# Kernel optimization log

Hardware: AMD Instinct MI355X
Metric: run time of the kernel (lower is better)

Reference implementation:

```python
import jax, jax.numpy as jnp
import numpy as np

D_MODEL = 1024
NUM_HEADS = 16
NUM_KV_HEADS = 4
D_K = D_MODEL // NUM_HEADS              # 64
G = NUM_HEADS // NUM_KV_HEADS           # queries per kv head = 4
B, S = 2, 2048


def setup_inputs() -> dict:
    key = jax.random.key(0)
    ks = jax.random.split(key, 11)
    s = 0.02
    return {
        "query": jax.random.normal(ks[0], (B, S, D_MODEL), jnp.float32),
        "key_in": jax.random.normal(ks[1], (B, S, D_MODEL), jnp.float32),
        "value_in": jax.random.normal(ks[2], (B, S, D_MODEL), jnp.float32),
        "Wq": jax.random.normal(ks[3], (D_MODEL, D_MODEL), jnp.float32) * s,
        "bq": jnp.zeros((D_MODEL,), jnp.float32),
        "Wk": jax.random.normal(ks[4], (D_MODEL, NUM_KV_HEADS * D_K), jnp.float32) * s,
        "bk": jnp.zeros((NUM_KV_HEADS * D_K,), jnp.float32),
        "Wv": jax.random.normal(ks[5], (D_MODEL, NUM_KV_HEADS * D_K), jnp.float32) * s,
        "bv": jnp.zeros((NUM_KV_HEADS * D_K,), jnp.float32),
        "Wo": jax.random.normal(ks[6], (D_MODEL, D_MODEL), jnp.float32) * s,
        "bo": jnp.zeros((D_MODEL,), jnp.float32),
    }


def reference(query, key_in, value_in, Wq, bq, Wk, bk, Wv, bv, Wo, bo):
    scale = jnp.sqrt(jnp.asarray(D_K, query.dtype))
    # Projections
    Q = (query @ Wq + bq).reshape(B, S, NUM_HEADS, D_K).transpose(0, 2, 1, 3)        # [B,H,S,dk]
    K = (key_in @ Wk + bk).reshape(B, S, NUM_KV_HEADS, D_K).transpose(0, 2, 1, 3)    # [B,KVH,S,dk]
    V = (value_in @ Wv + bv).reshape(B, S, NUM_KV_HEADS, D_K).transpose(0, 2, 1, 3)  # [B,KVH,S,dk]
    # repeat_interleave over head dim -> group Q heads by KV head instead
    Qg = Q.reshape(B, NUM_KV_HEADS, G, S, D_K)                                       # [B,KVH,G,S,dk]
    scores = jnp.einsum('bkgqd,bksd->bkgqs', Qg, K) / scale                          # [B,KVH,G,S,S]
    attn = jax.nn.softmax(scores, axis=-1)
    ctx = jnp.einsum('bkgqs,bksd->bkgqd', attn, V)                                   # [B,KVH,G,S,dk]
    ctx = ctx.reshape(B, NUM_HEADS, S, D_K).transpose(0, 2, 1, 3).reshape(B, S, D_MODEL)
    output = ctx @ Wo + bo
    # new_cache: K[:, ::G] on the repeated tensor == original K/V per kv head
    return output, K, V
```

## Files before the change

kernel.cpp:

```cpp
#include <hip/hip_runtime.h>

typedef unsigned short u16;
typedef unsigned int u32;
typedef __attribute__((ext_vector_type(8))) short short8;
typedef __attribute__((ext_vector_type(4))) float f32x4;

#define MFMA16(a, b, c) __builtin_amdgcn_mfma_f32_16x16x32_bf16(a, b, c, 0, 0, 0)

#define SEQ 2048
#define DM 1024

__device__ __forceinline__ u16 f2bf(float f) {
  u32 u = __float_as_uint(f);
  u += 0x7fffu + ((u >> 16) & 1u);
  return (u16)(u >> 16);
}
__device__ __forceinline__ u32 pack2(float a, float b) {
  u32 r;
  asm("v_cvt_pk_bf16_f32 %0, %1, %2" : "=v"(r) : "v"(a), "v"(b));
  return r;
}
__device__ __forceinline__ u32 pack2t(float a, float b) {
  return __builtin_amdgcn_perm(__float_as_uint(b), __float_as_uint(a), 0x07060302u);
}
__device__ __forceinline__ void pswap32(u32& a, u32& b) {
  asm("v_permlane32_swap_b32 %0, %1" : "+v"(a), "+v"(b));
}
__device__ __forceinline__ void pswap16(u32& a, u32& b) {
  asm("v_permlane16_swap_b32 %0, %1" : "+v"(a), "+v"(b));
}
__device__ __forceinline__ uint4 cvt8(const float* f) {
  float4 a = *(const float4*)f;
  float4 b = *(const float4*)(f + 4);
  uint4 r;
  r.x = pack2(a.x, a.y);
  r.y = pack2(a.z, a.w);
  r.z = pack2(b.x, b.y);
  r.w = pack2(b.z, b.w);
  return r;
}
__device__ __forceinline__ void gload16(const u16* g, u16* l) {
  __builtin_amdgcn_global_load_lds((const __attribute__((address_space(1))) u32*)g,
                                   (__attribute__((address_space(3))) u32*)l, 16, 0, 0);
}

__global__ void k_tr(const float* __restrict__ Wq, const float* __restrict__ Wk,
                     const float* __restrict__ Wv, const float* __restrict__ Wo,
                     u16* __restrict__ WqT, u16* __restrict__ WkT, u16* __restrict__ WvT,
                     u16* __restrict__ WoT) {
  const int z = blockIdx.z;
  const float* W = z == 0 ? Wq : (z == 1 ? Wk : (z == 2 ? Wv : Wo));
  u16* Wt = z == 0 ? WqT : (z == 1 ? WkT : (z == 2 ? WvT : WoT));
  const int N = (z == 1 || z == 2) ? 256 : 1024;
  const int n0 = blockIdx.x * 32;
  if (n0 >= N) return;
  const int k0 = blockIdx.y * 32;
  __shared__ float tile[32][33];
  int x = threadIdx.x & 31, y = threadIdx.x >> 5;
#pragma unroll
  for (int i = 0; i < 4; i++)
    tile[y + i * 8][x] = W[(size_t)(k0 + y + i * 8) * N + n0 + x];
  __syncthreads();
#pragma unroll
  for (int i = 0; i < 4; i++)
    Wt[(size_t)(n0 + y + i * 8) * 1024 + k0 + x] = f2bf(tile[x][y + i * 8]);
}

template <bool A32, bool B32>
__device__ __forceinline__ void gemm64(const void* __restrict__ A, const void* __restrict__ Bt,
                                       int m0, int n0, u16* lA, u16* lB, f32x4 acc[2][4]) {
  const int tid = threadIdx.x;
  const int lane = tid & 63, wave = tid >> 6;
  const int l15 = lane & 15, quad = lane >> 4;
  const int wm = wave >> 1, wn = wave & 1;
  const int sr = tid >> 3, scol = (tid & 7) * 8;
  f32x4 zero = {0.f, 0.f, 0.f, 0.f};
#pragma unroll
  for (int i = 0; i < 2; i++)
#pragma unroll
    for (int j = 0; j < 4; j++) acc[i][j] = zero;

  for (int k0 = 0; k0 < 1024; k0 += 64) {
    if constexpr (A32) {
      const float* Af = (const float*)A;
#pragma unroll
      for (int it = 0; it < 2; it++) {
        int r = sr + it * 32;
        uint4 v = cvt8(Af + (size_t)(m0 + r) * 1024 + k0 + scol);
        *(uint4*)&lA[r * 64 + (((tid & 7) ^ (r & 7)) << 3)] = v;
      }
    } else {
      const u16* Ab = (const u16*)A;
#pragma unroll
      for (int it = 0; it < 2; it++) {
        int w8 = wave * 2 + it;
        int r = w8 * 8 + (lane >> 3);
        int g = (lane & 7) ^ (lane >> 3);
        gload16(Ab + (size_t)(m0 + r) * 1024 + k0 + g * 8, &lA[w8 * 512]);
      }
    }
    if constexpr (B32) {
      const float* Bf = (const float*)Bt;
#pragma unroll
      for (int it = 0; it < 4; it++) {
        int r = sr + it * 32;
        uint4 v = cvt8(Bf + (size_t)(n0 + r) * 1024 + k0 + scol);
        *(uint4*)&lB[r * 64 + (((tid & 7) ^ (r & 7)) << 3)] = v;
      }
    } else {
      const u16* Bb = (const u16*)Bt;
#pragma unroll
      for (int it = 0; it < 4; it++) {
        int w8 = wave * 4 + it;
        int r = w8 * 8 + (lane >> 3);
        int g = (lane & 7) ^ (lane >> 3);
        gload16(Bb + (size_t)(n0 + r) * 1024 + k0 + g * 8, &lB[w8 * 512]);
      }
    }
    __syncthreads();
    short8 af[2][2], bfr[4][2];
#pragma unroll
    for (int i = 0; i < 2; i++)
#pragma unroll
      for (int kb = 0; kb < 2; kb++) {
        int r = wm * 32 + i * 16 + l15;
        af[i][kb] = *(const short8*)&lA[r * 64 + (((kb * 4 + quad) ^ (r & 7)) << 3)];
      }
#pragma unroll
    for (int j = 0; j < 4; j++)
#pragma unroll
      for (int kb = 0; kb < 2; kb++) {
        int r = wn * 64 + j * 16 + l15;
        bfr[j][kb] = *(const short8*)&lB[r * 64 + (((kb * 4 + quad) ^ (r & 7)) << 3)];
      }
#pragma unroll
    for (int i = 0; i < 2; i++)
#pragma unroll
      for (int j = 0; j < 4; j++) {
        acc[i][j] = MFMA16(af[i][0], bfr[j][0], acc[i][j]);
        acc[i][j] = MFMA16(af[i][1], bfr[j][1], acc[i][j]);
      }
    __syncthreads();
  }
}

__global__ __launch_bounds__(256) void k_proj(
    const float* __restrict__ query, const float* __restrict__ key_in,
    const float* __restrict__ value_in, const u16* __restrict__ WqT,
    const u16* __restrict__ WkT, const u16* __restrict__ WvT, const float* __restrict__ bq,
    const float* __restrict__ bk, const float* __restrict__ bv, u16* __restrict__ qbf,
    float* __restrict__ outK, u16* __restrict__ kbf, float* __restrict__ outV,
    u16* __restrict__ vtb, float qscale) {
  __shared__ u16 lA[64 * 64];
  __shared__ u16 lB[128 * 64];
  const int idx = blockIdx.x;
  const int lane = threadIdx.x & 63, wave = threadIdx.x >> 6;
  const int l15 = lane & 15, quad = lane >> 4;
  const int wm = wave >> 1, wn = wave & 1;
  f32x4 acc[2][4];

  if (idx < 640) {
    const u16* Wt;
    const float* act;
    const float* bias;
    int m0, n0, mode;
    if (idx < 512) {
      Wt = WqT; act = query; bias = bq; m0 = (idx >> 5) * 64; n0 = (idx & 31) * 128; mode = 0;
    } else {
      int i2 = idx - 512;
      Wt = WkT; act = key_in; bias = bk; m0 = (i2 >> 5) * 64; n0 = (i2 & 31) * 128; mode = 1;
    }
    gemm64<false, true>(Wt, act, m0, n0, lA, lB, acc);
#pragma unroll
    for (int i = 0; i < 2; i++) {
      int c0 = m0 + wm * 32 + i * 16 + quad * 4;
      float4 bb = *(const float4*)(bias + c0);
#pragma unroll
      for (int j = 0; j < 4; j++) {
        int token = n0 + wn * 64 + j * 16 + l15;
        int b = token >> 11, s = token & 2047;
        float v0 = acc[i][j][0] + bb.x, v1 = acc[i][j][1] + bb.y;
        float v2 = acc[i][j][2] + bb.z, v3 = acc[i][j][3] + bb.w;
        int d = c0 & 63;
        if (mode == 0) {
          int h = c0 >> 6;
          uint2 o;
          o.x = pack2(v0 * qscale, v1 * qscale);
          o.y = pack2(v2 * qscale, v3 * qscale);
          *(uint2*)(qbf + (((size_t)(b * 16 + h) * SEQ + s) << 6) + d) = o;
        } else {
          int kvh = c0 >> 6;
          size_t ix = (((size_t)(b * 4 + kvh) * SEQ + s) << 6) + d;
          float4 vv = {v0, v1, v2, v3};
          *(float4*)(outK + ix) = vv;
          uint2 o;
          o.x = pack2(v0, v1);
          o.y = pack2(v2, v3);
          *(uint2*)(kbf + ix) = o;
        }
      }
    }
  } else {
    int i2 = idx - 640;
    int m0 = (i2 >> 1) * 64, n0 = (i2 & 1) * 128;
    gemm64<true, false>(value_in, WvT, m0, n0, lA, lB, acc);
#pragma unroll
    for (int i = 0; i < 2; i++) {
      int r0 = m0 + wm * 32 + i * 16 + quad * 4;
      int b = r0 >> 11, s0 = r0 & 2047;
#pragma unroll
      for (int j = 0; j < 4; j++) {
        int col = n0 + wn * 64 + j * 16 + l15;
        int kvh = col >> 6, d = col & 63;
        float bv_ = bv[col];
        float v0 = acc[i][j][0] + bv_, v1 = acc[i][j][1] + bv_;
        float v2 = acc[i][j][2] + bv_, v3 = acc[i][j][3] + bv_;
        size_t base = (((size_t)(b * 4 + kvh) * SEQ + s0) << 6) + d;
        outV[base] = v0;
        outV[base + 64] = v1;
        outV[base + 128] = v2;
        outV[base + 192] = v3;
        uint2 o;
        o.x = pack2(v0, v1);
        o.y = pack2(v2, v3);
        *(uint2*)(vtb + ((size_t)(b * 4 + kvh) * 64 + d) * SEQ + s0) = o;
      }
    }
  }
}

__global__ __launch_bounds__(256) void k_out(const u16* __restrict__ ctxb,
                                             const u16* __restrict__ WoT,
                                             const float* __restrict__ bo,
                                             float* __restrict__ out) {
  __shared__ u16 lA[64 * 64];
  __shared__ u16 lB[128 * 64];
  const int idx = blockIdx.x;
  const int m0 = (idx >> 5) * 64, n0 = (idx & 31) * 128;
  const int lane = threadIdx.x & 63, wave = threadIdx.x >> 6;
  const int l15 = lane & 15, quad = lane >> 4;
  const int wm = wave >> 1, wn = wave & 1;
  f32x4 acc[2][4];
  gemm64<false, false>(WoT, ctxb, m0, n0, lA, lB, acc);
#pragma unroll
  for (int i = 0; i < 2; i++) {
    int c0 = m0 + wm * 32 + i * 16 + quad * 4;
    float4 bb = *(const float4*)(bo + c0);
#pragma unroll
    for (int j = 0; j < 4; j++) {
      int token = n0 + wn * 64 + j * 16 + l15;
      float4 vv = {acc[i][j][0] + bb.x, acc[i][j][1] + bb.y, acc[i][j][2] + bb.z,
                   acc[i][j][3] + bb.w};
      *(float4*)(out + (size_t)token * DM + c0) = vv;
    }
  }
}

__global__ __launch_bounds__(256, 2) void k_flash(const u16* __restrict__ Qh,
                                                  const u16* __restrict__ Kb,
                                                  const u16* __restrict__ Vt,
                                                  u16* __restrict__ ctx) {
  __shared__ u16 lK[2][128 * 64];
  __shared__ u16 lV[2][64 * 128];
  const int tid = threadIdx.x;
  const int lane = tid & 63, wave = tid >> 6;
  const int l15 = lane & 15, quad = lane >> 4;
  const int bh = blockIdx.y;
  const int b = bh >> 4, h = bh & 15, kvh = h >> 2;
  const u16* Q = Qh + (size_t)bh * SEQ * 64;
  const u16* Kp = Kb + (size_t)(b * 4 + kvh) * SEQ * 64;
  const u16* Vp = Vt + (size_t)(b * 4 + kvh) * 64 * SEQ;
  const int q0 = blockIdx.x * 128 + wave * 32;

  short8 qf[2][2];
#pragma unroll
  for (int g = 0; g < 2; g++)
#pragma unroll
    for (int kb = 0; kb < 2; kb++)
      qf[g][kb] = *(const short8*)(Q + (size_t)(q0 + g * 16 + l15) * 64 + kb * 32 + quad * 8);

  short8 ones8;
  {
    short ov = (l15 == 0) ? (short)0x3F80 : (short)0;
    ones8 = (short8){ov, ov, ov, ov, ov, ov, ov, ov};
  }

  f32x4 zero = {0.f, 0.f, 0.f, 0.f};
  f32x4 acc[2][4];
  f32x4 lacc[2] = {zero, zero};
#pragma unroll
  for (int g = 0; g < 2; g++)
#pragma unroll
    for (int n = 0; n < 4; n++) acc[g][n] = zero;

  const int gr3 = lane >> 3, gc7 = lane & 7;
  const int gr4 = lane >> 4, gc15 = lane & 15;

  auto stage = [&](int kc, int bufi) {
    u16* dK = lK[bufi];
    u16* dV = lV[bufi];
#pragma unroll
    for (int i = 0; i < 4; i++) {
      int slab = wave * 4 + i;
      gload16(Kp + (size_t)(kc + slab * 8 + gr3) * 64 + ((gc7 ^ gr3) << 3), dK + slab * 512);
    }
#pragma unroll
    for (int i = 0; i < 4; i++) {
      int slab = wave * 4 + i;
      int row = slab * 4 + gr4;
      gload16(Vp + (size_t)row * SEQ + kc + ((gc15 ^ (row & 15)) << 3), dV + slab * 512);
    }
  };

  stage(0, 0);
  __syncthreads();

  for (int t = 0; t < SEQ / 128; t++) {
    if (t < SEQ / 128 - 1) stage((t + 1) * 128, (t + 1) & 1);
    const u16* cK = lK[t & 1];
    const u16* cV = lV[t & 1];

#pragma unroll
    for (int sub = 0; sub < 2; sub++) {
      const int ks = sub * 64;
      f32x4 sc[2][4];
#pragma unroll
      for (int mt = 0; mt < 4; mt++) {
        int row = ks + mt * 16 + l15;
        short8 kf0 = *(const short8*)&cK[row * 64 + ((quad ^ (row & 7)) << 3)];
        short8 kf1 = *(const short8*)&cK[row * 64 + (((4 + quad) ^ (row & 7)) << 3)];
#pragma unroll
        for (int g = 0; g < 2; g++) {
          f32x4 t0 = MFMA16(kf0, qf[g][0], zero);
          sc[g][mt] = MFMA16(kf1, qf[g][1], t0);
        }
      }
#pragma unroll
      for (int g = 0; g < 2; g++)
#pragma unroll
        for (int mt = 0; mt < 4; mt++)
#pragma unroll
          for (int r = 0; r < 4; r++) sc[g][mt][r] = __builtin_amdgcn_exp2f(sc[g][mt][r]);

#pragma unroll
      for (int kbp = 0; kbp < 2; kbp++) {
        short8 pf[2];
#pragma unroll
        for (int g = 0; g < 2; g++) {
          u32 U0 = pack2t(sc[g][2 * kbp][0], sc[g][2 * kbp][1]);
          u32 W0 = pack2t(sc[g][2 * kbp + 1][0], sc[g][2 * kbp + 1][1]);
          u32 U1 = pack2t(sc[g][2 * kbp][2], sc[g][2 * kbp][3]);
          u32 W1 = pack2t(sc[g][2 * kbp + 1][2], sc[g][2 * kbp + 1][3]);
          pswap32(U0, W0);
          pswap16(U0, W0);
          pswap32(U1, W1);
          pswap16(U1, W1);
          u32 w[4] = {U0, U1, W0, W1};
          pf[g] = *(const short8*)w;
        }
        lacc[0] = MFMA16(ones8, pf[0], lacc[0]);
        lacc[1] = MFMA16(ones8, pf[1], lacc[1]);
#pragma unroll
        for (int n = 0; n < 4; n++) {
          int row = n * 16 + l15;
          int chv = sub * 8 + kbp * 4 + quad;
          short8 vf = *(const short8*)&cV[row * 128 + ((chv ^ (row & 15)) << 3)];
          acc[0][n] = MFMA16(vf, pf[0], acc[0][n]);
          acc[1][n] = MFMA16(vf, pf[1], acc[1][n]);
        }
      }
    }
    __syncthreads();
  }

#pragma unroll
  for (int g = 0; g < 2; g++) {
    float lq = __shfl(lacc[g][0], l15);
    float inv = __builtin_amdgcn_rcpf(lq);
    u16* base = ctx + ((size_t)(b * SEQ + q0 + g * 16 + l15)) * DM + h * 64;
#pragma unroll
    for (int n = 0; n < 4; n++) {
      uint2 o;
      o.x = pack2t(acc[g][n][0] * inv, acc[g][n][1] * inv);
      o.y = pack2t(acc[g][n][2] * inv, acc[g][n][3] * inv);
      *(uint2*)(base + n * 16 + quad * 4) = o;
    }
  }
}

extern "C" void kernel_launch(void* const* d_in, const int* in_sizes, int n_in,
                              void* d_out, int out_size, void* d_ws, size_t ws_size,
                              hipStream_t stream) {
  const float* query = (const float*)d_in[0];
  const float* key_in = (const float*)d_in[1];
  const float* value_in = (const float*)d_in[2];
  const float* Wq = (const float*)d_in[3];
  const float* bq = (const float*)d_in[4];
  const float* Wk = (const float*)d_in[5];
  const float* bk = (const float*)d_in[6];
  const float* Wv = (const float*)d_in[7];
  const float* bv = (const float*)d_in[8];
  const float* Wo = (const float*)d_in[9];
  const float* bo = (const float*)d_in[10];

  float* out = (float*)d_out;
  float* outK = out + 4194304;
  float* outV = out + 5242880;

  char* ws = (char*)d_ws;
  u16* WqT = (u16*)(ws);
  u16* WkT = (u16*)(ws + 2097152);
  u16* WvT = (u16*)(ws + 2621440);
  u16* WoT = (u16*)(ws + 3145728);
  u16* qbf = (u16*)(ws + 5242880);
  u16* kbf = (u16*)(ws + 13631488);
  u16* vtb = (u16*)(ws + 15728640);
  u16* ctxb = (u16*)(ws + 17825792);

  const float qscale = 0.125f * 1.44269504088896340736f;

  k_tr<<<dim3(32, 32, 4), 256, 0, stream>>>(Wq, Wk, Wv, Wo, WqT, WkT, WvT, WoT);
  k_proj<<<dim3(768), 256, 0, stream>>>(query, key_in, value_in, WqT, WkT, WvT, bq, bk, bv,
                                        qbf, outK, kbf, outV, vtb, qscale);
  k_flash<<<dim3(16, 32), 256, 0, stream>>>(qbf, kbf, vtb, ctxb);
  k_out<<<dim3(512), 256, 0, stream>>>(ctxb, WoT, bo, out);
}
```

Baseline: 200.1 us.

## Fuse weight transpose into GEMM loads and double-buffer LDS tiles

Drops the separate weight transpose/bf16-convert kernel. The projection and output GEMMs now read fp32 weights directly with strided loads, converting and transposing them while writing to LDS. The GEMM main loop is also double-buffered: the next tile's global loads go into registers before the MFMAs on the current tile, and are written to LDS afterwards. This saves one launch and one pass over the weights, at the cost of more registers, twice the LDS, and less coalesced weight reads, since each lane reads one column across rows.

```diff
diff --git a/kernel.cpp b/kernel.cpp
--- a/kernel.cpp
+++ b/kernel.cpp
@@ -10,11 +10,6 @@
 #define SEQ 2048
 #define DM 1024
 
-__device__ __forceinline__ u16 f2bf(float f) {
-  u32 u = __float_as_uint(f);
-  u += 0x7fffu + ((u >> 16) & 1u);
-  return (u16)(u >> 16);
-}
 __device__ __forceinline__ u32 pack2(float a, float b) {
   u32 r;
   asm("v_cvt_pk_bf16_f32 %0, %1, %2" : "=v"(r) : "v"(a), "v"(b));
@@ -29,109 +24,152 @@
 __device__ __forceinline__ void pswap16(u32& a, u32& b) {
   asm("v_permlane16_swap_b32 %0, %1" : "+v"(a), "+v"(b));
 }
-__device__ __forceinline__ uint4 cvt8(const float* f) {
-  float4 a = *(const float4*)f;
-  float4 b = *(const float4*)(f + 4);
-  uint4 r;
-  r.x = pack2(a.x, a.y);
-  r.y = pack2(a.z, a.w);
-  r.z = pack2(b.x, b.y);
-  r.w = pack2(b.z, b.w);
-  return r;
-}
 __device__ __forceinline__ void gload16(const u16* g, u16* l) {
   __builtin_amdgcn_global_load_lds((const __attribute__((address_space(1))) u32*)g,
                                    (__attribute__((address_space(3))) u32*)l, 16, 0, 0);
 }
 
-__global__ void k_tr(const float* __restrict__ Wq, const float* __restrict__ Wk,
-                     const float* __restrict__ Wv, const float* __restrict__ Wo,
-                     u16* __restrict__ WqT, u16* __restrict__ WkT, u16* __restrict__ WvT,
-                     u16* __restrict__ WoT) {
-  const int z = blockIdx.z;
-  const float* W = z == 0 ? Wq : (z == 1 ? Wk : (z == 2 ? Wv : Wo));
-  u16* Wt = z == 0 ? WqT : (z == 1 ? WkT : (z == 2 ? WvT : WoT));
-  const int N = (z == 1 || z == 2) ? 256 : 1024;
-  const int n0 = blockIdx.x * 32;
-  if (n0 >= N) return;
-  const int k0 = blockIdx.y * 32;
-  __shared__ float tile[32][33];
-  int x = threadIdx.x & 31, y = threadIdx.x >> 5;
-#pragma unroll
-  for (int i = 0; i < 4; i++)
-    tile[y + i * 8][x] = W[(size_t)(k0 + y + i * 8) * N + n0 + x];
-  __syncthreads();
-#pragma unroll
-  for (int i = 0; i < 4; i++)
-    Wt[(size_t)(n0 + y + i * 8) * 1024 + k0 + x] = f2bf(tile[x][y + i * 8]);
-}
-
-template <bool A32, bool B32>
-__device__ __forceinline__ void gemm64(const void* __restrict__ A, const void* __restrict__ Bt,
-                                       int m0, int n0, u16* lA, u16* lB, f32x4 acc[2][4]) {
+#define MBF 0
+#define MF32 1
+#define MTR 2
+
+template <int AM, int BM>
+__device__ __forceinline__ void gemm64(const void* __restrict__ A, const void* __restrict__ B,
+                                       int m0, int n0, int ldA, int ldB, u16* lA, u16* lB,
+                                       f32x4 acc[2][4]) {
   const int tid = threadIdx.x;
   const int lane = tid & 63, wave = tid >> 6;
   const int l15 = lane & 15, quad = lane >> 4;
   const int wm = wave >> 1, wn = wave & 1;
-  const int sr = tid >> 3, scol = (tid & 7) * 8;
+  const int sr = tid >> 3, sch = tid & 7;
+  const int gr = lane >> 3, gch = (lane & 7) ^ (lane >> 3);
+  const int nb = tid & 127, ko = tid >> 7;
   f32x4 zero = {0.f, 0.f, 0.f, 0.f};
 #pragma unroll
   for (int i = 0; i < 2; i++)
 #pragma unroll
     for (int j = 0; j < 4; j++) acc[i][j] = zero;
 
-  for (int k0 = 0; k0 < 1024; k0 += 64) {
-    if constexpr (A32) {
-      const float* Af = (const float*)A;
+  float rA[16], rB[32];
+
+  auto issue = [&](int k0, u16* dA, u16* dB) {
+    if constexpr (AM == MBF) {
+#pragma unroll
+      for (int it = 0; it < 2; it++) {
+        int w8 = wave * 2 + it;
+        gload16((const u16*)A + (size_t)(m0 + w8 * 8 + gr) * ldA + k0 + gch * 8,
+                dA + w8 * 512);
+      }
+    } else if constexpr (AM == MF32) {
+#pragma unroll
+      for (int it = 0; it < 2; it++) {
+        const float* p = (const float*)A + (size_t)(m0 + sr + it * 32) * ldA + k0 + sch * 8;
+        float4 a = *(const float4*)p, b = *(const float4*)(p + 4);
+        rA[it * 8 + 0] = a.x; rA[it * 8 + 1] = a.y; rA[it * 8 + 2] = a.z; rA[it * 8 + 3] = a.w;
+        rA[it * 8 + 4] = b.x; rA[it * 8 + 5] = b.y; rA[it * 8 + 6] = b.z; rA[it * 8 + 7] = b.w;
+      }
+    } else {
+      const float* Wf = (const float*)A;
+#pragma unroll
+      for (int j = 0; j < 16; j++)
+        rA[j] = Wf[(size_t)(k0 + wave * 16 + j) * ldA + m0 + lane];
+    }
+    if constexpr (BM == MBF) {
+#pragma unroll
+      for (int it = 0; it < 4; it++) {
+        int w8 = wave * 4 + it;
+        gload16((const u16*)B + (size_t)(n0 + w8 * 8 + gr) * ldB + k0 + gch * 8,
+                dB + w8 * 512);
+      }
+    } else if constexpr (BM == MF32) {
+#pragma unroll
+      for (int it = 0; it < 4; it++) {
+        const float* p = (const float*)B + (size_t)(n0 + sr + it * 32) * ldB + k0 + sch * 8;
+        float4 a = *(const float4*)p, b = *(const float4*)(p + 4);
+        rB[it * 8 + 0] = a.x; rB[it * 8 + 1] = a.y; rB[it * 8 + 2] = a.z; rB[it * 8 + 3] = a.w;
+        rB[it * 8 + 4] = b.x; rB[it * 8 + 5] = b.y; rB[it * 8 + 6] = b.z; rB[it * 8 + 7] = b.w;
+      }
+    } else {
+      const float* Wf = (const float*)B;
+#pragma unroll
+      for (int j = 0; j < 32; j++)
+        rB[j] = Wf[(size_t)(k0 + ko * 32 + j) * ldB + n0 + nb];
+    }
+  };
+
+  auto wrb = [&](u16* dA, u16* dB) {
+    if constexpr (AM == MF32) {
 #pragma unroll
       for (int it = 0; it < 2; it++) {
         int r = sr + it * 32;
-        uint4 v = cvt8(Af + (size_t)(m0 + r) * 1024 + k0 + scol);
-        *(uint4*)&lA[r * 64 + (((tid & 7) ^ (r & 7)) << 3)] = v;
-      }
-    } else {
-      const u16* Ab = (const u16*)A;
-#pragma unroll
-      for (int it = 0; it < 2; it++) {
-        int w8 = wave * 2 + it;
-        int r = w8 * 8 + (lane >> 3);
-        int g = (lane & 7) ^ (lane >> 3);
-        gload16(Ab + (size_t)(m0 + r) * 1024 + k0 + g * 8, &lA[w8 * 512]);
-      }
-    }
-    if constexpr (B32) {
-      const float* Bf = (const float*)Bt;
+        uint4 v;
+        v.x = pack2(rA[it * 8 + 0], rA[it * 8 + 1]);
+        v.y = pack2(rA[it * 8 + 2], rA[it * 8 + 3]);
+        v.z = pack2(rA[it * 8 + 4], rA[it * 8 + 5]);
+        v.w = pack2(rA[it * 8 + 6], rA[it * 8 + 7]);
+        *(uint4*)&dA[r * 64 + ((sch ^ (r & 7)) << 3)] = v;
+      }
+    } else if constexpr (AM == MTR) {
+#pragma unroll
+      for (int o = 0; o < 2; o++) {
+        uint4 v;
+        v.x = pack2(rA[o * 8 + 0], rA[o * 8 + 1]);
+        v.y = pack2(rA[o * 8 + 2], rA[o * 8 + 3]);
+        v.z = pack2(rA[o * 8 + 4], rA[o * 8 + 5]);
+        v.w = pack2(rA[o * 8 + 6], rA[o * 8 + 7]);
+        int c = (wave * 2 + o) ^ (lane & 7);
+        *(uint4*)&dA[lane * 64 + (c << 3)] = v;
+      }
+    }
+    if constexpr (BM == MF32) {
 #pragma unroll
       for (int it = 0; it < 4; it++) {
         int r = sr + it * 32;
-        uint4 v = cvt8(Bf + (size_t)(n0 + r) * 1024 + k0 + scol);
-        *(uint4*)&lB[r * 64 + (((tid & 7) ^ (r & 7)) << 3)] = v;
-      }
-    } else {
-      const u16* Bb = (const u16*)Bt;
-#pragma unroll
-      for (int it = 0; it < 4; it++) {
-        int w8 = wave * 4 + it;
-        int r = w8 * 8 + (lane >> 3);
-        int g = (lane & 7) ^ (lane >> 3);
-        gload16(Bb + (size_t)(n0 + r) * 1024 + k0 + g * 8, &lB[w8 * 512]);
-      }
-    }
-    __syncthreads();
+        uint4 v;
+        v.x = pack2(rB[it * 8 + 0], rB[it * 8 + 1]);
+        v.y = pack2(rB[it * 8 + 2], rB[it * 8 + 3]);
+        v.z = pack2(rB[it * 8 + 4], rB[it * 8 + 5]);
+        v.w = pack2(rB[it * 8 + 6], rB[it * 8 + 7]);
+        *(uint4*)&dB[r * 64 + ((sch ^ (r & 7)) << 3)] = v;
+      }
+    } else if constexpr (BM == MTR) {
+#pragma unroll
+      for (int o = 0; o < 4; o++) {
+        uint4 v;
+        v.x = pack2(rB[o * 8 + 0], rB[o * 8 + 1]);
+        v.y = pack2(rB[o * 8 + 2], rB[o * 8 + 3]);
+        v.z = pack2(rB[o * 8 + 4], rB[o * 8 + 5]);
+        v.w = pack2(rB[o * 8 + 6], rB[o * 8 + 7]);
+        int c = (ko * 4 + o) ^ (nb & 7);
+        *(uint4*)&dB[nb * 64 + (c << 3)] = v;
+      }
+    }
+  };
+
+  issue(0, lA, lB);
+  wrb(lA, lB);
+  __syncthreads();
+
+  for (int t = 0; t < 16; t++) {
+    u16* cA = lA + (t & 1) * 4096;
+    u16* cB = lB + (t & 1) * 8192;
+    u16* nA = lA + ((t + 1) & 1) * 4096;
+    u16* nB = lB + ((t + 1) & 1) * 8192;
+    if (t < 15) issue((t + 1) * 64, nA, nB);
     short8 af[2][2], bfr[4][2];
 #pragma unroll
     for (int i = 0; i < 2; i++)
 #pragma unroll
       for (int kb = 0; kb < 2; kb++) {
         int r = wm * 32 + i * 16 + l15;
-        af[i][kb] = *(const short8*)&lA[r * 64 + (((kb * 4 + quad) ^ (r & 7)) << 3)];
+        af[i][kb] = *(const short8*)&cA[r * 64 + (((kb * 4 + quad) ^ (r & 7)) << 3)];
       }
 #pragma unroll
     for (int j = 0; j < 4; j++)
 #pragma unroll
       for (int kb = 0; kb < 2; kb++) {
         int r = wn * 64 + j * 16 + l15;
-        bfr[j][kb] = *(const short8*)&lB[r * 64 + (((kb * 4 + quad) ^ (r & 7)) << 3)];
+        bfr[j][kb] = *(const short8*)&cB[r * 64 + (((kb * 4 + quad) ^ (r & 7)) << 3)];
       }
 #pragma unroll
     for (int i = 0; i < 2; i++)
@@ -140,19 +178,20 @@
         acc[i][j] = MFMA16(af[i][0], bfr[j][0], acc[i][j]);
         acc[i][j] = MFMA16(af[i][1], bfr[j][1], acc[i][j]);
       }
+    if (t < 15) wrb(nA, nB);
     __syncthreads();
   }
 }
 
-__global__ __launch_bounds__(256) void k_proj(
+__global__ __launch_bounds__(256, 3) void k_proj(
     const float* __restrict__ query, const float* __restrict__ key_in,
-    const float* __restrict__ value_in, const u16* __restrict__ WqT,
-    const u16* __restrict__ WkT, const u16* __restrict__ WvT, const float* __restrict__ bq,
+    const float* __restrict__ value_in, const float* __restrict__ Wq,
+    const float* __restrict__ Wk, const float* __restrict__ Wv, const float* __restrict__ bq,
     const float* __restrict__ bk, const float* __restrict__ bv, u16* __restrict__ qbf,
     float* __restrict__ outK, u16* __restrict__ kbf, float* __restrict__ outV,
     u16* __restrict__ vtb, float qscale) {
-  __shared__ u16 lA[64 * 64];
-  __shared__ u16 lB[128 * 64];
+  __shared__ u16 lA[2 * 4096];
+  __shared__ u16 lB[2 * 8192];
   const int idx = blockIdx.x;
   const int lane = threadIdx.x & 63, wave = threadIdx.x >> 6;
   const int l15 = lane & 15, quad = lane >> 4;
@@ -160,17 +199,19 @@
   f32x4 acc[2][4];
 
   if (idx < 640) {
-    const u16* Wt;
+    const float* Wt;
     const float* act;
     const float* bias;
-    int m0, n0, mode;
+    int m0, n0, ldW, mode;
     if (idx < 512) {
-      Wt = WqT; act = query; bias = bq; m0 = (idx >> 5) * 64; n0 = (idx & 31) * 128; mode = 0;
+      Wt = Wq; act = query; bias = bq; ldW = 1024;
+      m0 = (idx >> 5) * 64; n0 = (idx & 31) * 128; mode = 0;
     } else {
       int i2 = idx - 512;
-      Wt = WkT; act = key_in; bias = bk; m0 = (i2 >> 5) * 64; n0 = (i2 & 31) * 128; mode = 1;
-    }
-    gemm64<false, true>(Wt, act, m0, n0, lA, lB, acc);
+      Wt = Wk; act = key_in; bias = bk; ldW = 256;
+      m0 = (i2 >> 5) * 64; n0 = (i2 & 31) * 128; mode = 1;
+    }
+    gemm64<MTR, MF32>(Wt, act, m0, n0, ldW, 1024, lA, lB, acc);
 #pragma unroll
     for (int i = 0; i < 2; i++) {
       int c0 = m0 + wm * 32 + i * 16 + quad * 4;
@@ -203,7 +244,7 @@
   } else {
     int i2 = idx - 640;
     int m0 = (i2 >> 1) * 64, n0 = (i2 & 1) * 128;
-    gemm64<true, false>(value_in, WvT, m0, n0, lA, lB, acc);
+    gemm64<MF32, MTR>(value_in, Wv, m0, n0, 1024, 256, lA, lB, acc);
 #pragma unroll
     for (int i = 0; i < 2; i++) {
       int r0 = m0 + wm * 32 + i * 16 + quad * 4;
@@ -229,19 +270,19 @@
   }
 }
 
-__global__ __launch_bounds__(256) void k_out(const u16* __restrict__ ctxb,
-                                             const u16* __restrict__ WoT,
-                                             const float* __restrict__ bo,
-                                             float* __restrict__ out) {
-  __shared__ u16 lA[64 * 64];
-  __shared__ u16 lB[128 * 64];
+__global__ __launch_bounds__(256, 2) void k_out(const u16* __restrict__ ctxb,
+                                                const float* __restrict__ Wo,
+                                                const float* __restrict__ bo,
+                                                float* __restrict__ out) {
+  __shared__ u16 lA[2 * 4096];
+  __shared__ u16 lB[2 * 8192];
   const int idx = blockIdx.x;
   const int m0 = (idx >> 5) * 64, n0 = (idx & 31) * 128;
   const int lane = threadIdx.x & 63, wave = threadIdx.x >> 6;
   const int l15 = lane & 15, quad = lane >> 4;
   const int wm = wave >> 1, wn = wave & 1;
   f32x4 acc[2][4];
-  gemm64<false, false>(WoT, ctxb, m0, n0, lA, lB, acc);
+  gemm64<MTR, MBF>(Wo, ctxb, m0, n0, 1024, 1024, lA, lB, acc);
 #pragma unroll
   for (int i = 0; i < 2; i++) {
     int c0 = m0 + wm * 32 + i * 16 + quad * 4;
@@ -408,10 +449,6 @@
   float* outV = out + 5242880;
 
   char* ws = (char*)d_ws;
-  u16* WqT = (u16*)(ws);
-  u16* WkT = (u16*)(ws + 2097152);
-  u16* WvT = (u16*)(ws + 2621440);
-  u16* WoT = (u16*)(ws + 3145728);
   u16* qbf = (u16*)(ws + 5242880);
   u16* kbf = (u16*)(ws + 13631488);
   u16* vtb = (u16*)(ws + 15728640);
@@ -419,9 +456,8 @@
 
   const float qscale = 0.125f * 1.44269504088896340736f;
 
-  k_tr<<<dim3(32, 32, 4), 256, 0, stream>>>(Wq, Wk, Wv, Wo, WqT, WkT, WvT, WoT);
-  k_proj<<<dim3(768), 256, 0, stream>>>(query, key_in, value_in, WqT, WkT, WvT, bq, bk, bv,
+  k_proj<<<dim3(768), 256, 0, stream>>>(query, key_in, value_in, Wq, Wk, Wv, bq, bk, bv,
                                         qbf, outK, kbf, outV, vtb, qscale);
   k_flash<<<dim3(16, 32), 256, 0, stream>>>(qbf, kbf, vtb, ctxb);
-  k_out<<<dim3(512), 256, 0, stream>>>(ctxb, WoT, bo, out);
-}
+  k_out<<<dim3(512), 256, 0, stream>>>(ctxb, Wo, bo, out);
+}
```

Measured after the change: 218.0 us. 9.0% more time.
